# Kernel optimization log

Measured on AMD Instinct MI355X. Metric: run time of the kernel, lower is better.

The kernel has to match this reference:

```python
import jax, jax.numpy as jnp
import numpy as np

B, C, H, W = 4, 64, 64, 64
INTER = max(1, C // 8)


def setup_inputs() -> dict:
    key = jax.random.key(0)
    ks = jax.random.split(key, 8)
    return {
        "x": jax.random.normal(ks[0], (B, C, H, W), dtype=jnp.float32),
        "Wq": jax.random.normal(ks[1], (INTER, C), dtype=jnp.float32) * 0.1,
        "bq": jax.random.normal(ks[2], (INTER,), dtype=jnp.float32) * 0.1,
        "Wk": jax.random.normal(ks[3], (INTER, C), dtype=jnp.float32) * 0.1,
        "bk": jax.random.normal(ks[4], (INTER,), dtype=jnp.float32) * 0.1,
        "Wv": jax.random.normal(ks[5], (C, C), dtype=jnp.float32) * 0.1,
        "bv": jax.random.normal(ks[6], (C,), dtype=jnp.float32) * 0.1,
        "gamma": jax.random.normal(ks[7], (1,), dtype=jnp.float32),
    }


def reference(x, Wq, bq, Wk, bk, Wv, bv, gamma):
    b, c, h, w = x.shape
    n = h * w
    xf = x.reshape(b, c, n)  # flatten spatial dims, [B, C, N]
    # 1x1 convs == per-pixel matmuls
    q = jnp.einsum('ic,bcn->bin', Wq, xf) + bq[None, :, None]  # [B, inter, N]
    k = jnp.einsum('ic,bcn->bin', Wk, xf) + bk[None, :, None]  # [B, inter, N]
    v = jnp.einsum('oc,bcn->bon', Wv, xf) + bv[None, :, None]  # [B, C, N]
    # energy[b,n,m] = sum_i q[b,i,n] * k[b,i,m]  (unscaled attention)
    energy = jnp.einsum('bin,bim->bnm', q, k)  # [B, N, N]
    attn = jax.nn.softmax(energy, axis=-1)
    # out[b,c,n] = sum_m v[b,c,m] * attn[b,n,m]
    out = jnp.einsum('bcm,bnm->bcn', v, attn).reshape(b, c, h, w)
    return gamma[0] * out + x
```

## Files before the change

kernel.cpp:

```cpp
#include <hip/hip_runtime.h>


#define NPIX 4096
typedef __attribute__((ext_vector_type(8))) short s8v;
typedef __attribute__((ext_vector_type(4))) float f4v;

static __device__ __forceinline__ unsigned short f2bf(float f) {
    union { float f; unsigned u; } v; v.f = f;
    unsigned r = v.u + 0x7FFFu + ((v.u >> 16) & 1u);
    return (unsigned short)(r >> 16);
}

extern "C" __global__ void __launch_bounds__(256) qkv_kernel(
    const float* __restrict__ x,
    const float* __restrict__ Wq, const float* __restrict__ bq,
    const float* __restrict__ Wk, const float* __restrict__ bk,
    const float* __restrict__ Wv, const float* __restrict__ bv,
    unsigned short* __restrict__ qt, unsigned short* __restrict__ kt,
    unsigned short* __restrict__ vb)
{
    __shared__ float xs[64][17];
    __shared__ __align__(16) float wls[80][68];
    __shared__ float bls[80];
    const int t = threadIdx.x;
    const int b = blockIdx.x >> 8, n0 = (blockIdx.x & 255) << 4;

    for (int e = t; e < 1024; e += 256) {
        int c = e >> 4, j = e & 15;
        xs[c][j] = x[((b << 6) + c) * NPIX + n0 + j];
    }
    for (int e = t; e < 5120; e += 256) {
        int row = e >> 6, cc = e & 63;
        wls[row][cc] = (e < 512) ? Wq[e] : (e < 1024) ? Wk[e - 512] : Wv[e - 1024];
    }
    if (t < 80) bls[t] = (t < 8) ? bq[t] : (t < 16) ? bk[t - 8] : bv[t - 16];
    __syncthreads();

    const int j = t & 15, oh = t >> 4;
    float xr[64];
#pragma unroll
    for (int c = 0; c < 64; ++c) xr[c] = xs[c][j];

    const int n = n0 + j;
#pragma unroll
    for (int r = 0; r < 5; ++r) {
        const int row = oh * 5 + r;
        float acc = bls[row];
#pragma unroll
        for (int q = 0; q < 16; ++q) {
            float4 wv = *(const float4*)&wls[row][q * 4];
            acc += wv.x * xr[4*q] + wv.y * xr[4*q+1] + wv.z * xr[4*q+2] + wv.w * xr[4*q+3];
        }
        const unsigned short h = f2bf(acc);
        if (row < 8)       qt[(b * NPIX + n) * 8 + row] = h;
        else if (row < 16) kt[(b * NPIX + n) * 8 + row - 8] = h;
        else               vb[((b << 6) + (row - 16)) * NPIX + n] = h;
    }
}

template<int S, bool DIRECT>
__global__ __launch_bounds__(256) void attn_kern(
    const unsigned short* __restrict__ qt, const unsigned short* __restrict__ kt,
    const unsigned short* __restrict__ vb,
    const float* __restrict__ x, const float* __restrict__ gamma_p,
    float* __restrict__ out, float* __restrict__ Opart, float* __restrict__ Lpart)
{
    constexpr int LS = (S == 1) ? 0 : (S == 2) ? 1 : 2;
    constexpr int TC = 64 / S;

    __shared__ __align__(16) unsigned short vls[64][64];
    __shared__ __align__(16) unsigned short pls[4][16][72];
    __shared__ float lls[4][16];

    const int t = threadIdx.x;
    const int w = t >> 6, lane = t & 63, g = lane >> 4, c16 = lane & 15;
    const int bid = blockIdx.x;
    const int s  = bid & (S - 1);
    const int nt = (bid >> LS) & 63;
    const int b  = bid >> (LS + 6);
    const int n0 = nt << 6;
    const int tb = s * TC;

    const unsigned short* qtB = qt + b * NPIX * 8;
    const unsigned short* ktB = kt + b * NPIX * 8;
    const unsigned short* vbB = vb + (b << 6) * NPIX;

    s8v qfr = {0,0,0,0,0,0,0,0};
    if (g == 0) qfr = *(const s8v*)(qtB + (n0 + w * 16 + c16) * 8);

    const int vc = t >> 2, vq = t & 3;
    const int p0 = (2 * vq)     ^ (vc & 7);
    const int p1 = (2 * vq + 1) ^ (vc & 7);

    f4v accO[4];
#pragma unroll
    for (int cs = 0; cs < 4; ++cs) { accO[cs][0]=0.f; accO[cs][1]=0.f; accO[cs][2]=0.f; accO[cs][3]=0.f; }
    float lsum[4] = {0.f, 0.f, 0.f, 0.f};

    s8v vr0, vr1, kf[4], kfn[4];
    {
        const int m0 = tb << 6;
        const unsigned short* vp = vbB + vc * NPIX + m0 + vq * 16;
        vr0 = *(const s8v*)(vp);
        vr1 = *(const s8v*)(vp + 8);
#pragma unroll
        for (int ms = 0; ms < 4; ++ms) {
            s8v z = {0,0,0,0,0,0,0,0};
            kf[ms] = z;
            if (g == 0) kf[ms] = *(const s8v*)(ktB + (m0 + ms * 16 + c16) * 8);
        }
    }

    for (int ti = 0; ti < TC; ++ti) {
        *(s8v*)&vls[vc][p0 * 8] = vr0;
        *(s8v*)&vls[vc][p1 * 8] = vr1;
        __syncthreads();

        if (ti < TC - 1) {
            const int m1 = (tb + ti + 1) << 6;
            const unsigned short* vp = vbB + vc * NPIX + m1 + vq * 16;
            vr0 = *(const s8v*)(vp);
            vr1 = *(const s8v*)(vp + 8);
#pragma unroll
            for (int ms = 0; ms < 4; ++ms) {
                s8v z = {0,0,0,0,0,0,0,0};
                kfn[ms] = z;
                if (g == 0) kfn[ms] = *(const s8v*)(ktB + (m1 + ms * 16 + c16) * 8);
            }
        }

        f4v sm[4];
#pragma unroll
        for (int ms = 0; ms < 4; ++ms) {
            f4v z; z[0]=0.f; z[1]=0.f; z[2]=0.f; z[3]=0.f;
            sm[ms] = __builtin_amdgcn_mfma_f32_16x16x32_bf16(qfr, kf[ms], z, 0, 0, 0);
        }

#pragma unroll
        for (int ms = 0; ms < 4; ++ms)
#pragma unroll
            for (int r = 0; r < 4; ++r) {
                float p = __expf(sm[ms][r]);
                lsum[r] += p;
                pls[w][g * 4 + r][ms * 16 + c16] = f2bf(p);
            }
        __builtin_amdgcn_wave_barrier();

        s8v pf0 = *(const s8v*)&pls[w][c16][g * 8];
        s8v pf1 = *(const s8v*)&pls[w][c16][32 + g * 8];

#pragma unroll
        for (int cs = 0; cs < 4; ++cs) {
            const int c = cs * 16 + c16;
            const int q0 = (g)     ^ (c16 & 7);
            const int q1 = (4 + g) ^ (c16 & 7);
            s8v vf0 = *(const s8v*)&vls[c][q0 * 8];
            s8v vf1 = *(const s8v*)&vls[c][q1 * 8];
            accO[cs] = __builtin_amdgcn_mfma_f32_16x16x32_bf16(vf0, pf0, accO[cs], 0, 0, 0);
            accO[cs] = __builtin_amdgcn_mfma_f32_16x16x32_bf16(vf1, pf1, accO[cs], 0, 0, 0);
        }
        __syncthreads();

#pragma unroll
        for (int ms = 0; ms < 4; ++ms) kf[ms] = kfn[ms];
    }

#pragma unroll
    for (int r = 0; r < 4; ++r) {
        float L = lsum[r];
        L += __shfl_xor(L, 1); L += __shfl_xor(L, 2);
        L += __shfl_xor(L, 4); L += __shfl_xor(L, 8);
        lsum[r] = L;
    }

    const int n = n0 + w * 16 + c16;
    if constexpr (DIRECT) {
        if (c16 == 0) {
#pragma unroll
            for (int r = 0; r < 4; ++r) lls[w][g * 4 + r] = lsum[r];
        }
        __builtin_amdgcn_wave_barrier();
        const float inv = 1.0f / lls[w][c16];
        const float gm = gamma_p[0];
#pragma unroll
        for (int cs = 0; cs < 4; ++cs)
#pragma unroll
            for (int r = 0; r < 4; ++r) {
                const int c = cs * 16 + g * 4 + r;
                const int gi = ((b << 6) + c) * NPIX + n;
                out[gi] = gm * (accO[cs][r] * inv) + x[gi];
            }
    } else {
        (void)lls;
#pragma unroll
        for (int cs = 0; cs < 4; ++cs)
#pragma unroll
            for (int r = 0; r < 4; ++r) {
                const int c = cs * 16 + g * 4 + r;
                Opart[((((s << 2) + b) << 6) + c) * NPIX + n] = accO[cs][r];
            }
        if (c16 == 0) {
#pragma unroll
            for (int r = 0; r < 4; ++r)
                Lpart[(((s << 2) + b) * NPIX) + n0 + w * 16 + g * 4 + r] = lsum[r];
        }
    }
}

template<int S>
__global__ __launch_bounds__(256) void combine_kern(
    const float* __restrict__ Opart, const float* __restrict__ Lpart,
    const float* __restrict__ x, const float* __restrict__ gamma_p,
    float* __restrict__ out)
{
    const int tid = blockIdx.x * 256 + threadIdx.x;
    const int e = tid << 2;
    const int n = e & 4095, c = (e >> 12) & 63, b = e >> 18;
    float4 o = {0.f,0.f,0.f,0.f}, l = {0.f,0.f,0.f,0.f};
#pragma unroll
    for (int s = 0; s < S; ++s) {
        float4 ov = *(const float4*)&Opart[((((s << 2) + b) << 6) + c) * NPIX + n];
        float4 lv = *(const float4*)&Lpart[(((s << 2) + b) * NPIX) + n];
        o.x += ov.x; o.y += ov.y; o.z += ov.z; o.w += ov.w;
        l.x += lv.x; l.y += lv.y; l.z += lv.z; l.w += lv.w;
    }
    const float gm = gamma_p[0];
    float4 xv = *(const float4*)&x[e];
    float4 r;
    r.x = gm * o.x / l.x + xv.x;
    r.y = gm * o.y / l.y + xv.y;
    r.z = gm * o.z / l.z + xv.z;
    r.w = gm * o.w / l.w + xv.w;
    *(float4*)&out[e] = r;
}

extern "C" void kernel_launch(void* const* d_in, const int* in_sizes, int n_in,
                              void* d_out, int out_size, void* d_ws, size_t ws_size,
                              hipStream_t stream) {
    const float* x     = (const float*)d_in[0];
    const float* Wq    = (const float*)d_in[1];
    const float* bq    = (const float*)d_in[2];
    const float* Wk    = (const float*)d_in[3];
    const float* bk    = (const float*)d_in[4];
    const float* Wv    = (const float*)d_in[5];
    const float* bv    = (const float*)d_in[6];
    const float* gamma = (const float*)d_in[7];

    unsigned short* qt = (unsigned short*)d_ws;
    unsigned short* kt = qt + 4 * NPIX * 8;
    unsigned short* vb = kt + 4 * NPIX * 8;
    float* Opart = (float*)(vb + 4 * 64 * NPIX);
    const size_t base = (size_t)(4 * NPIX * 8) * 2 * 2 + (size_t)4 * 64 * NPIX * 2;
    const size_t per_slice = (size_t)4 * 64 * NPIX * 4 + (size_t)4 * NPIX * 4;

    float* out = (float*)d_out;
    qkv_kernel<<<1024, 256, 0, stream>>>(x, Wq, bq, Wk, bk, Wv, bv, qt, kt, vb);

    if (ws_size >= base + 4 * per_slice) {
        float* Lpart = Opart + (size_t)4 * 4 * 64 * NPIX;
        attn_kern<4, false><<<1024, 256, 0, stream>>>(qt, kt, vb, x, gamma, out, Opart, Lpart);
        combine_kern<4><<<1024, 256, 0, stream>>>(Opart, Lpart, x, gamma, out);
    } else if (ws_size >= base + 2 * per_slice) {
        float* Lpart = Opart + (size_t)2 * 4 * 64 * NPIX;
        attn_kern<2, false><<<512, 256, 0, stream>>>(qt, kt, vb, x, gamma, out, Opart, Lpart);
        combine_kern<2><<<1024, 256, 0, stream>>>(Opart, Lpart, x, gamma, out);
    } else {
        attn_kern<1, true><<<256, 256, 0, stream>>>(qt, kt, vb, x, gamma, out, nullptr, nullptr);
    }
}
```

Measured before the change: 114.7 us.

## Replace split-KV plus combine kernel with in-block key split and shared-memory reduction

The attention kernel now uses 512-thread blocks covering 32 query pixels. Four wave-pair groups each process a quarter of the keys, and their partial outputs and row sums are reduced through shared memory, so the Opart/Lpart global round trip and the separate combine kernel go away. Block indices are remapped to interleave batch/tile assignment, and launch bounds now set a minimum occupancy. In exchange each V/K tile serves only 32 queries instead of 64, which doubles global reads of V and K, and the reduction adds extra barriers plus more shared memory per block.

```diff
diff --git a/kernel.cpp b/kernel.cpp
--- a/kernel.cpp
+++ b/kernel.cpp
@@ -11,7 +11,7 @@
     return (unsigned short)(r >> 16);
 }
 
-extern "C" __global__ void __launch_bounds__(256) qkv_kernel(
+extern "C" __global__ void __launch_bounds__(256, 4) qkv_kernel(
     const float* __restrict__ x,
     const float* __restrict__ Wq, const float* __restrict__ bq,
     const float* __restrict__ Wk, const float* __restrict__ bk,
@@ -58,69 +58,65 @@
     }
 }
 
-template<int S, bool DIRECT>
-__global__ __launch_bounds__(256) void attn_kern(
+extern "C" __global__ void __launch_bounds__(512, 4) attn_kernel(
     const unsigned short* __restrict__ qt, const unsigned short* __restrict__ kt,
     const unsigned short* __restrict__ vb,
     const float* __restrict__ x, const float* __restrict__ gamma_p,
-    float* __restrict__ out, float* __restrict__ Opart, float* __restrict__ Lpart)
+    float* __restrict__ out)
 {
-    constexpr int LS = (S == 1) ? 0 : (S == 2) ? 1 : 2;
-    constexpr int TC = 64 / S;
-
-    __shared__ __align__(16) unsigned short vls[64][64];
-    __shared__ __align__(16) unsigned short pls[4][16][72];
-    __shared__ float lls[4][16];
+    __shared__ __align__(16) unsigned short vls[4][64][64];
+    __shared__ __align__(16) unsigned short pls[8][16][72];
+    __shared__ float ored[2][128][17];
+    __shared__ float Lred[4][2][16];
 
     const int t = threadIdx.x;
     const int w = t >> 6, lane = t & 63, g = lane >> 4, c16 = lane & 15;
-    const int bid = blockIdx.x;
-    const int s  = bid & (S - 1);
-    const int nt = (bid >> LS) & 63;
-    const int b  = bid >> (LS + 6);
-    const int n0 = nt << 6;
-    const int tb = s * TC;
+    const int gg = w >> 1, wg = w & 1;
+    const int bid = ((blockIdx.x & 7) << 6) + (blockIdx.x >> 3);
+    const int b = bid >> 7, n0 = (bid & 127) << 5;
 
     const unsigned short* qtB = qt + b * NPIX * 8;
     const unsigned short* ktB = kt + b * NPIX * 8;
     const unsigned short* vbB = vb + (b << 6) * NPIX;
 
     s8v qfr = {0,0,0,0,0,0,0,0};
-    if (g == 0) qfr = *(const s8v*)(qtB + (n0 + w * 16 + c16) * 8);
-
-    const int vc = t >> 2, vq = t & 3;
-    const int p0 = (2 * vq)     ^ (vc & 7);
-    const int p1 = (2 * vq + 1) ^ (vc & 7);
+    if (g == 0) qfr = *(const s8v*)(qtB + (n0 + wg * 16 + c16) * 8);
+
+    const int t2 = t & 127;
+    const int vc = t2 >> 1, hh = t2 & 1;
+    const int mbase = gg << 10;
 
     f4v accO[4];
 #pragma unroll
     for (int cs = 0; cs < 4; ++cs) { accO[cs][0]=0.f; accO[cs][1]=0.f; accO[cs][2]=0.f; accO[cs][3]=0.f; }
     float lsum[4] = {0.f, 0.f, 0.f, 0.f};
 
-    s8v vr0, vr1, kf[4], kfn[4];
+    s8v vr[4], kf[4], kfn[4];
     {
-        const int m0 = tb << 6;
-        const unsigned short* vp = vbB + vc * NPIX + m0 + vq * 16;
-        vr0 = *(const s8v*)(vp);
-        vr1 = *(const s8v*)(vp + 8);
+        const unsigned short* vp = vbB + vc * NPIX + mbase + hh * 32;
+        vr[0] = *(const s8v*)(vp);     vr[1] = *(const s8v*)(vp + 8);
+        vr[2] = *(const s8v*)(vp + 16); vr[3] = *(const s8v*)(vp + 24);
 #pragma unroll
         for (int ms = 0; ms < 4; ++ms) {
             s8v z = {0,0,0,0,0,0,0,0};
             kf[ms] = z;
-            if (g == 0) kf[ms] = *(const s8v*)(ktB + (m0 + ms * 16 + c16) * 8);
-        }
-    }
-
-    for (int ti = 0; ti < TC; ++ti) {
-        *(s8v*)&vls[vc][p0 * 8] = vr0;
-        *(s8v*)&vls[vc][p1 * 8] = vr1;
+            if (g == 0) kf[ms] = *(const s8v*)(ktB + (mbase + ms * 16 + c16) * 8);
+        }
+    }
+
+    for (int ti = 0; ti < 16; ++ti) {
+#pragma unroll
+        for (int q = 0; q < 4; ++q) {
+            const int pos = (hh * 4 + q) ^ (vc & 7);
+            *(s8v*)&vls[gg][vc][pos * 8] = vr[q];
+        }
         __syncthreads();
 
-        if (ti < TC - 1) {
-            const int m1 = (tb + ti + 1) << 6;
-            const unsigned short* vp = vbB + vc * NPIX + m1 + vq * 16;
-            vr0 = *(const s8v*)(vp);
-            vr1 = *(const s8v*)(vp + 8);
+        if (ti < 15) {
+            const int m1 = mbase + ((ti + 1) << 6);
+            const unsigned short* vp = vbB + vc * NPIX + m1 + hh * 32;
+            vr[0] = *(const s8v*)(vp);      vr[1] = *(const s8v*)(vp + 8);
+            vr[2] = *(const s8v*)(vp + 16); vr[3] = *(const s8v*)(vp + 24);
 #pragma unroll
             for (int ms = 0; ms < 4; ++ms) {
                 s8v z = {0,0,0,0,0,0,0,0};
@@ -154,8 +150,8 @@
             const int c = cs * 16 + c16;
             const int q0 = (g)     ^ (c16 & 7);
             const int q1 = (4 + g) ^ (c16 & 7);
-            s8v vf0 = *(const s8v*)&vls[c][q0 * 8];
-            s8v vf1 = *(const s8v*)&vls[c][q1 * 8];
+            s8v vf0 = *(const s8v*)&vls[gg][c][q0 * 8];
+            s8v vf1 = *(const s8v*)&vls[gg][c][q1 * 8];
             accO[cs] = __builtin_amdgcn_mfma_f32_16x16x32_bf16(vf0, pf0, accO[cs], 0, 0, 0);
             accO[cs] = __builtin_amdgcn_mfma_f32_16x16x32_bf16(vf1, pf1, accO[cs], 0, 0, 0);
         }
@@ -172,16 +168,44 @@
         L += __shfl_xor(L, 4); L += __shfl_xor(L, 8);
         lsum[r] = L;
     }
-
-    const int n = n0 + w * 16 + c16;
-    if constexpr (DIRECT) {
-        if (c16 == 0) {
-#pragma unroll
-            for (int r = 0; r < 4; ++r) lls[w][g * 4 + r] = lsum[r];
-        }
-        __builtin_amdgcn_wave_barrier();
-        const float inv = 1.0f / lls[w][c16];
+    if (c16 == 0) {
+#pragma unroll
+        for (int r = 0; r < 4; ++r) Lred[gg][wg][g * 4 + r] = lsum[r];
+    }
+
+    const int s2 = t & 127;
+    if (gg >= 2) {
+#pragma unroll
+        for (int cs = 0; cs < 4; ++cs)
+#pragma unroll
+            for (int r = 0; r < 4; ++r) ored[gg - 2][s2][cs * 4 + r] = accO[cs][r];
+    }
+    __syncthreads();
+    if (gg < 2) {
+#pragma unroll
+        for (int cs = 0; cs < 4; ++cs)
+#pragma unroll
+            for (int r = 0; r < 4; ++r) accO[cs][r] += ored[gg][s2][cs * 4 + r];
+    }
+    __syncthreads();
+    if (gg == 1) {
+#pragma unroll
+        for (int cs = 0; cs < 4; ++cs)
+#pragma unroll
+            for (int r = 0; r < 4; ++r) ored[0][s2][cs * 4 + r] = accO[cs][r];
+    }
+    __syncthreads();
+    if (gg == 0) {
+#pragma unroll
+        for (int cs = 0; cs < 4; ++cs)
+#pragma unroll
+            for (int r = 0; r < 4; ++r) accO[cs][r] += ored[0][s2][cs * 4 + r];
+
+        const float L = Lred[0][wg][c16] + Lred[1][wg][c16]
+                      + Lred[2][wg][c16] + Lred[3][wg][c16];
+        const float inv = 1.0f / L;
         const float gm = gamma_p[0];
+        const int n = n0 + wg * 16 + c16;
 #pragma unroll
         for (int cs = 0; cs < 4; ++cs)
 #pragma unroll
@@ -190,48 +214,7 @@
                 const int gi = ((b << 6) + c) * NPIX + n;
                 out[gi] = gm * (accO[cs][r] * inv) + x[gi];
             }
-    } else {
-        (void)lls;
-#pragma unroll
-        for (int cs = 0; cs < 4; ++cs)
-#pragma unroll
-            for (int r = 0; r < 4; ++r) {
-                const int c = cs * 16 + g * 4 + r;
-                Opart[((((s << 2) + b) << 6) + c) * NPIX + n] = accO[cs][r];
-            }
-        if (c16 == 0) {
-#pragma unroll
-            for (int r = 0; r < 4; ++r)
-                Lpart[(((s << 2) + b) * NPIX) + n0 + w * 16 + g * 4 + r] = lsum[r];
-        }
-    }
-}
-
-template<int S>
-__global__ __launch_bounds__(256) void combine_kern(
-    const float* __restrict__ Opart, const float* __restrict__ Lpart,
-    const float* __restrict__ x, const float* __restrict__ gamma_p,
-    float* __restrict__ out)
-{
-    const int tid = blockIdx.x * 256 + threadIdx.x;
-    const int e = tid << 2;
-    const int n = e & 4095, c = (e >> 12) & 63, b = e >> 18;
-    float4 o = {0.f,0.f,0.f,0.f}, l = {0.f,0.f,0.f,0.f};
-#pragma unroll
-    for (int s = 0; s < S; ++s) {
-        float4 ov = *(const float4*)&Opart[((((s << 2) + b) << 6) + c) * NPIX + n];
-        float4 lv = *(const float4*)&Lpart[(((s << 2) + b) * NPIX) + n];
-        o.x += ov.x; o.y += ov.y; o.z += ov.z; o.w += ov.w;
-        l.x += lv.x; l.y += lv.y; l.z += lv.z; l.w += lv.w;
-    }
-    const float gm = gamma_p[0];
-    float4 xv = *(const float4*)&x[e];
-    float4 r;
-    r.x = gm * o.x / l.x + xv.x;
-    r.y = gm * o.y / l.y + xv.y;
-    r.z = gm * o.z / l.z + xv.z;
-    r.w = gm * o.w / l.w + xv.w;
-    *(float4*)&out[e] = r;
+    }
 }
 
 extern "C" void kernel_launch(void* const* d_in, const int* in_sizes, int n_in,
@@ -249,22 +232,7 @@
     unsigned short* qt = (unsigned short*)d_ws;
     unsigned short* kt = qt + 4 * NPIX * 8;
     unsigned short* vb = kt + 4 * NPIX * 8;
-    float* Opart = (float*)(vb + 4 * 64 * NPIX);
-    const size_t base = (size_t)(4 * NPIX * 8) * 2 * 2 + (size_t)4 * 64 * NPIX * 2;
-    const size_t per_slice = (size_t)4 * 64 * NPIX * 4 + (size_t)4 * NPIX * 4;
-
-    float* out = (float*)d_out;
+
     qkv_kernel<<<1024, 256, 0, stream>>>(x, Wq, bq, Wk, bk, Wv, bv, qt, kt, vb);
-
-    if (ws_size >= base + 4 * per_slice) {
-        float* Lpart = Opart + (size_t)4 * 4 * 64 * NPIX;
-        attn_kern<4, false><<<1024, 256, 0, stream>>>(qt, kt, vb, x, gamma, out, Opart, Lpart);
-        combine_kern<4><<<1024, 256, 0, stream>>>(Opart, Lpart, x, gamma, out);
-    } else if (ws_size >= base + 2 * per_slice) {
-        float* Lpart = Opart + (size_t)2 * 4 * 64 * NPIX;
-        attn_kern<2, false><<<512, 256, 0, stream>>>(qt, kt, vb, x, gamma, out, Opart, Lpart);
-        combine_kern<2><<<1024, 256, 0, stream>>>(Opart, Lpart, x, gamma, out);
-    } else {
-        attn_kern<1, true><<<256, 256, 0, stream>>>(qt, kt, vb, x, gamma, out, nullptr, nullptr);
-    }
-}
+    attn_kernel<<<512, 512, 0, stream>>>(qt, kt, vb, x, gamma, (float*)d_out);
+}
```

Result: faster. 112.0 us (-2.3%).
